# Kernel tuning notes

Hardware: AMD Instinct MI355X
Metric: run time of the kernel (lower is better)

The kernel has to match this reference:

```python
import jax, jax.numpy as jnp
import numpy as np

B, S, K, D = 64, 2048, 256, 512


def setup_inputs() -> dict:
    key = jax.random.key(0)
    kx, kw = jax.random.split(key)
    x = jax.random.normal(kx, (B, S, K), dtype=jnp.float32)
    dataMinor = jax.random.normal(kw, (K, D), dtype=jnp.float32)
    return {"x": x, "dataMinor": dataMinor}


def reference(x, dataMinor):
    # Faithful math: mean_s(x @ W). Since mean and the contraction commute,
    # reduce over seq first, then one small GEMM (same result, fewer FLOPs).
    # x: [B, S, K]; dataMinor: [K, D] -> out: [B, D]
    x_mean = jnp.mean(x, axis=1)            # [B, K]
    return jnp.einsum('bk,kd->bd', x_mean, dataMinor)
```

## Files before the change

### kernel.cpp

```cpp
#include <hip/hip_runtime.h>


typedef float f32x4 __attribute__((ext_vector_type(4)));

#define BB 64
#define SS 2048
#define KK 256
#define DD 512
#define CHUNKS 16
#define RPC (SS / CHUNKS)
#define NBLK (BB * CHUNKS)
#define NXCD 8

__global__ __launch_bounds__(256) void partial_sum_kernel(const float* __restrict__ x,
                                                          float* __restrict__ part) {
    const int virt = (blockIdx.x & (NXCD - 1)) * (NBLK / NXCD) + (blockIdx.x >> 3);
    const int b  = virt >> 4;
    const int c  = virt & 15;
    const int t  = threadIdx.x;
    const int tx = t & 63;
    const int ty = t >> 6;

    const f32x4* xp = (const f32x4*)(x + ((size_t)b * SS + (size_t)c * RPC) * KK) + tx;

    f32x4 acc = {0.f, 0.f, 0.f, 0.f};
    #pragma unroll
    for (int i = 0; i < RPC / 4; ++i)
        acc += xp[(size_t)(i * 4 + ty) * (KK / 4)];

    __shared__ f32x4 smem[4][64];
    smem[ty][tx] = acc;
    __syncthreads();

    if (ty == 0) {
        f32x4 r = (smem[0][tx] + smem[1][tx]) + (smem[2][tx] + smem[3][tx]);
        ((f32x4*)(part + ((size_t)b * CHUNKS + c) * KK))[tx] = r;
    }
}

__global__ __launch_bounds__(256) void finish_kernel(const float* __restrict__ part,
                                                     const float* __restrict__ w,
                                                     float* __restrict__ out) {
    const int b  = blockIdx.x >> 2;
    const int dq = blockIdx.x & 3;
    const int t  = threadIdx.x;

    __shared__ float xm[KK];
    {
        float s = 0.f;
        const float* pp = part + (size_t)b * CHUNKS * KK + t;
        #pragma unroll
        for (int c = 0; c < CHUNKS; ++c) s += pp[c * KK];
        xm[t] = s * (1.0f / SS);
    }
    __syncthreads();

    const int col4 = dq * 32 + (t & 31);
    const int kg   = t >> 5;
    const f32x4* w4 = (const f32x4*)w;

    f32x4 acc = {0.f, 0.f, 0.f, 0.f};
    #pragma unroll
    for (int kk = 0; kk < 32; ++kk) {
        const int k = kg * 32 + kk;
        acc += xm[k] * w4[(size_t)k * (DD / 4) + col4];
    }

    __shared__ f32x4 red[8][32];
    if (kg) red[kg][t & 31] = acc;
    __syncthreads();
    if (kg == 0) {
        #pragma unroll
        for (int g = 1; g < 8; ++g) acc += red[g][t];
        ((f32x4*)out)[(size_t)b * (DD / 4) + col4] = acc;
    }
}

extern "C" void kernel_launch(void* const* d_in, const int* in_sizes, int n_in,
                              void* d_out, int out_size, void* d_ws, size_t ws_size,
                              hipStream_t stream) {
    const float* x = (const float*)d_in[0];
    const float* w = (const float*)d_in[1];
    float* out  = (float*)d_out;
    float* part = (float*)d_ws;

    partial_sum_kernel<<<NBLK, 256, 0, stream>>>(x, part);
    finish_kernel<<<BB * 4, 256, 0, stream>>>(part, w, out);
}
```

Baseline: 28.37 us.

## Fuse partial-sum and GEMV into one kernel with atomic accumulation and per-batch counters

Merges the two kernels into one launch: producer blocks atomically add their chunk sums into a per-batch accumulator and bump a per-batch counter. Consumer blocks, placed after the producers in the grid, spin on the counter and then run the small GEMV. This removes the second kernel launch and the partial buffer round trip. In exchange it adds a memset launch, float atomics that make the summation order nondeterministic, and spin-waiting that relies on producers being scheduled before consumers.

```diff
diff --git a/kernel.cpp b/kernel.cpp
--- a/kernel.cpp
+++ b/kernel.cpp
@@ -9,70 +9,76 @@
 #define DD 512
 #define CHUNKS 16
 #define RPC (SS / CHUNKS)
-#define NBLK (BB * CHUNKS)
+#define NPROD (BB * CHUNKS)
+#define NFIN (BB * 4)
 #define NXCD 8
 
-__global__ __launch_bounds__(256) void partial_sum_kernel(const float* __restrict__ x,
-                                                          float* __restrict__ part) {
-    const int virt = (blockIdx.x & (NXCD - 1)) * (NBLK / NXCD) + (blockIdx.x >> 3);
-    const int b  = virt >> 4;
-    const int c  = virt & 15;
-    const int t  = threadIdx.x;
-    const int tx = t & 63;
-    const int ty = t >> 6;
+__global__ __launch_bounds__(256) void fused_kernel(const float* __restrict__ x,
+                                                    const float* __restrict__ w,
+                                                    float* __restrict__ out,
+                                                    float* __restrict__ acc,
+                                                    unsigned int* __restrict__ cnt) {
+    const int t = threadIdx.x;
 
-    const f32x4* xp = (const f32x4*)(x + ((size_t)b * SS + (size_t)c * RPC) * KK) + tx;
+    if (blockIdx.x < NPROD) {
+        const int virt = (blockIdx.x & (NXCD - 1)) * (NPROD / NXCD) + (blockIdx.x >> 3);
+        const int b  = virt >> 4;
+        const int c  = virt & 15;
+        const int tx = t & 63;
+        const int ty = t >> 6;
 
-    f32x4 acc = {0.f, 0.f, 0.f, 0.f};
-    #pragma unroll
-    for (int i = 0; i < RPC / 4; ++i)
-        acc += xp[(size_t)(i * 4 + ty) * (KK / 4)];
+        const f32x4* xp = (const f32x4*)(x + ((size_t)b * SS + (size_t)c * RPC) * KK) + tx;
 
-    __shared__ f32x4 smem[4][64];
-    smem[ty][tx] = acc;
-    __syncthreads();
+        f32x4 a = {0.f, 0.f, 0.f, 0.f};
+        #pragma unroll
+        for (int i = 0; i < RPC / 4; ++i)
+            a += xp[(size_t)(i * 4 + ty) * (KK / 4)];
 
-    if (ty == 0) {
-        f32x4 r = (smem[0][tx] + smem[1][tx]) + (smem[2][tx] + smem[3][tx]);
-        ((f32x4*)(part + ((size_t)b * CHUNKS + c) * KK))[tx] = r;
-    }
-}
+        __shared__ float sm[4][KK];
+        *(f32x4*)&sm[ty][tx * 4] = a;
+        __syncthreads();
 
-__global__ __launch_bounds__(256) void finish_kernel(const float* __restrict__ part,
-                                                     const float* __restrict__ w,
-                                                     float* __restrict__ out) {
-    const int b  = blockIdx.x >> 2;
-    const int dq = blockIdx.x & 3;
-    const int t  = threadIdx.x;
+        const float v = (sm[0][t] + sm[1][t]) + (sm[2][t] + sm[3][t]);
+        atomicAdd(&acc[(size_t)b * KK + t], v);
+        asm volatile("s_waitcnt vmcnt(0)" ::: "memory");
+        __syncthreads();
+        if (t == 0) atomicAdd(&cnt[b], 1u);
+    } else {
+        const int wblk = blockIdx.x - NPROD;
+        const int b  = wblk >> 2;
+        const int dq = wblk & 3;
 
-    __shared__ float xm[KK];
-    {
-        float s = 0.f;
-        const float* pp = part + (size_t)b * CHUNKS * KK + t;
+        if (t == 0) {
+            while (__hip_atomic_load(&cnt[b], __ATOMIC_RELAXED, __HIP_MEMORY_SCOPE_AGENT)
+                   < (unsigned)CHUNKS)
+                __builtin_amdgcn_s_sleep(8);
+        }
+        __syncthreads();
+
+        __shared__ float xm[KK];
+        xm[t] = __hip_atomic_load(&acc[(size_t)b * KK + t], __ATOMIC_RELAXED,
+                                  __HIP_MEMORY_SCOPE_AGENT) * (1.0f / SS);
+        __syncthreads();
+
+        const int col4 = dq * 32 + (t & 31);
+        const int kg   = t >> 5;
+        const f32x4* w4 = (const f32x4*)w;
+
+        f32x4 o = {0.f, 0.f, 0.f, 0.f};
         #pragma unroll
-        for (int c = 0; c < CHUNKS; ++c) s += pp[c * KK];
-        xm[t] = s * (1.0f / SS);
-    }
-    __syncthreads();
+        for (int kk = 0; kk < 32; ++kk) {
+            const int k = kg * 32 + kk;
+            o += xm[k] * w4[(size_t)k * (DD / 4) + col4];
+        }
 
-    const int col4 = dq * 32 + (t & 31);
-    const int kg   = t >> 5;
-    const f32x4* w4 = (const f32x4*)w;
-
-    f32x4 acc = {0.f, 0.f, 0.f, 0.f};
-    #pragma unroll
-    for (int kk = 0; kk < 32; ++kk) {
-        const int k = kg * 32 + kk;
-        acc += xm[k] * w4[(size_t)k * (DD / 4) + col4];
-    }
-
-    __shared__ f32x4 red[8][32];
-    if (kg) red[kg][t & 31] = acc;
-    __syncthreads();
-    if (kg == 0) {
-        #pragma unroll
-        for (int g = 1; g < 8; ++g) acc += red[g][t];
-        ((f32x4*)out)[(size_t)b * (DD / 4) + col4] = acc;
+        __shared__ f32x4 red[8][32];
+        if (kg) red[kg][t & 31] = o;
+        __syncthreads();
+        if (kg == 0) {
+            #pragma unroll
+            for (int g = 1; g < 8; ++g) o += red[g][t];
+            ((f32x4*)out)[(size_t)b * (DD / 4) + col4] = o;
+        }
     }
 }
 
@@ -81,9 +87,10 @@
                               hipStream_t stream) {
     const float* x = (const float*)d_in[0];
     const float* w = (const float*)d_in[1];
-    float* out  = (float*)d_out;
-    float* part = (float*)d_ws;
+    float* out = (float*)d_out;
+    float* acc = (float*)d_ws;
+    unsigned int* cnt = (unsigned int*)(acc + BB * KK);
 
-    partial_sum_kernel<<<NBLK, 256, 0, stream>>>(x, part);
-    finish_kernel<<<BB * 4, 256, 0, stream>>>(part, w, out);
+    hipMemsetAsync(d_ws, 0, (BB * KK + BB) * sizeof(float), stream);
+    fused_kernel<<<NPROD + NFIN, 256, 0, stream>>>(x, w, out, acc, cnt);
 }
```

After: 43.82 us. +54.5%, slower.
